# Optimization experiments

Hardware: AMD Instinct MI355X
Metric: run time of the kernel (lower is better)

## Reference

```python
import jax, jax.numpy as jnp
import numpy as np

N = 100000   # nodes
E = 800000   # edges
F_IN = 128   # in_channels
C = 64       # out_channels
H = 2 * C    # hidden = 2*out_channels


def _w(key, shape, fan_in):
    return jax.random.normal(key, shape, jnp.float32) * (1.0 / np.sqrt(fan_in))


def setup_inputs() -> dict:
    key = jax.random.key(0)
    ks = jax.random.split(key, 12)
    return {
        "x": jax.random.normal(ks[0], (N, F_IN), jnp.float32),
        "edge_index": jax.random.randint(ks[1], (2, E), 0, N, dtype=jnp.int32),
        # layer 1 (F_IN -> H)
        "W1_in": _w(ks[2], (F_IN, H), F_IN),
        "W1_out": _w(ks[3], (F_IN, H), F_IN),
        "W1_root": _w(ks[4], (F_IN, H), F_IN),
        "b1": jnp.zeros((H,), jnp.float32),
        # layer 2 (H -> C)
        "W2_in": _w(ks[5], (H, C), H),
        "W2_out": _w(ks[6], (H, C), H),
        "W2_root": _w(ks[7], (H, C), H),
        "b2": jnp.zeros((C,), jnp.float32),
    }


def _gcn(x, W, src, dst):
    # GCNConv with add_self_loops=False, bias=None:
    # out[dst] += deg^-1/2[src] * deg^-1/2[dst] * (x @ W)[src]
    h = x @ W
    deg = jax.ops.segment_sum(jnp.ones_like(dst, jnp.float32), dst, num_segments=N)
    dinv = jnp.where(deg > 0, jax.lax.rsqrt(jnp.maximum(deg, 1.0)), 0.0)
    norm = dinv[src] * dinv[dst]                 # [E]
    msg = h[src] * norm[:, None]                 # [E, F_out]
    return jax.ops.segment_sum(msg, dst, num_segments=N)


def _dir_layer(x, W_in, W_out, W_root, b, src, dst, alpha=0.5):
    x_in = _gcn(x, W_in, src, dst)               # original direction
    x_out = _gcn(x, W_out, dst, src)             # flipped edges
    return alpha * x_out + (1.0 - alpha) * x_in + x @ W_root + b


def reference(x, edge_index, W1_in, W1_out, W1_root, b1, W2_in, W2_out, W2_root, b2):
    src, dst = edge_index[0], edge_index[1]
    h = jax.nn.relu(_dir_layer(x, W1_in, W1_out, W1_root, b1, src, dst))
    return _dir_layer(h, W2_in, W2_out, W2_root, b2, src, dst)
```

## Files before the change

### kernel.cpp

```cpp
#include <hip/hip_runtime.h>

typedef __attribute__((ext_vector_type(8))) short bf16x8;
typedef __attribute__((ext_vector_type(4))) float f32x4;

#define NB 196
#define CAP 8192
#define SBLK 256
#define ECH 3125
#define GEMM_BLOCKS 1563

__device__ __forceinline__ unsigned short f2bf(float f) {
    unsigned int u = __float_as_uint(f);
    u = (u + 0x7FFFu + ((u >> 16) & 1u)) >> 16;
    return (unsigned short)u;
}
__device__ __forceinline__ float bf2f(unsigned short v) {
    return __uint_as_float(((unsigned int)v) << 16);
}

__device__ __forceinline__ void gemm1_body(
    unsigned short* As, unsigned short* Bs, int bid,
    const float* __restrict__ Ag, const unsigned short* __restrict__ BTcat,
    const float* __restrict__ bias,
    unsigned short* __restrict__ Y0, unsigned short* __restrict__ Y1,
    unsigned short* __restrict__ Y2, int nrows)
{
    const int t  = threadIdx.x;
    const int w  = t >> 6, l = t & 63;
    const int g  = l >> 4, li = l & 15;
    const int wr = w >> 1, wc = w & 1;
    const int row0 = bid * 64;

    #pragma unroll
    for (int i = 0; i < 4; ++i) {
        const int q   = t + 256 * i;
        const int row = q >> 4;
        const int ck  = q & 15;
        unsigned short o[8];
        if (row0 + row < nrows) {
            const f32x4* src = (const f32x4*)(Ag + (size_t)(row0 + row) * 128 + ck * 8);
            const f32x4 a = __builtin_nontemporal_load(src);
            const f32x4 b = __builtin_nontemporal_load(src + 1);
            o[0]=f2bf(a.x); o[1]=f2bf(a.y); o[2]=f2bf(a.z); o[3]=f2bf(a.w);
            o[4]=f2bf(b.x); o[5]=f2bf(b.y); o[6]=f2bf(b.z); o[7]=f2bf(b.w);
        } else {
            #pragma unroll
            for (int u = 0; u < 8; ++u) o[u] = 0;
        }
        *(int4*)&As[row * 128 + ((ck ^ (row & 7)) << 3)] = *(int4*)o;
    }

    #pragma unroll 1
    for (int wgt = 0; wgt < 3; ++wgt) {
        __syncthreads();
        {
            const int4* Bg = (const int4*)(BTcat + (size_t)wgt * 128 * 128);
            #pragma unroll
            for (int i = 0; i < 8; ++i) {
                const int q   = t + 256 * i;
                const int row = q >> 4;
                const int ck  = q & 15;
                const int4 v  = Bg[q];
                *(int4*)&Bs[row * 128 + ((ck ^ (row & 7)) << 3)] = v;
            }
        }
        __syncthreads();

        f32x4 acc[2][4];
        #pragma unroll
        for (int rf = 0; rf < 2; ++rf)
            #pragma unroll
            for (int cf = 0; cf < 4; ++cf)
                acc[rf][cf] = (f32x4){0.f, 0.f, 0.f, 0.f};

        #pragma unroll
        for (int kk = 0; kk < 4; ++kk) {
            bf16x8 av[2], bv[4];
            #pragma unroll
            for (int rf = 0; rf < 2; ++rf) {
                const int ar = wr * 32 + rf * 16 + li;
                const int ck = (kk * 4 + g) ^ (ar & 7);
                av[rf] = *(const bf16x8*)&As[ar * 128 + (ck << 3)];
            }
            #pragma unroll
            for (int cf = 0; cf < 4; ++cf) {
                const int bc = wc * 64 + cf * 16 + li;
                const int ck = (kk * 4 + g) ^ (bc & 7);
                bv[cf] = *(const bf16x8*)&Bs[bc * 128 + (ck << 3)];
            }
            #pragma unroll
            for (int rf = 0; rf < 2; ++rf)
                #pragma unroll
                for (int cf = 0; cf < 4; ++cf)
                    acc[rf][cf] = __builtin_amdgcn_mfma_f32_16x16x32_bf16(
                        av[rf], bv[cf], acc[rf][cf], 0, 0, 0);
        }

        unsigned short* Y = (wgt == 0) ? Y0 : (wgt == 1) ? Y1 : Y2;
        #pragma unroll
        for (int rf = 0; rf < 2; ++rf) {
            #pragma unroll
            for (int i = 0; i < 4; ++i) {
                const int r = row0 + wr * 32 + rf * 16 + 4 * g + i;
                if (r < nrows) {
                    #pragma unroll
                    for (int cf = 0; cf < 4; ++cf) {
                        const int c = wc * 64 + cf * 16 + li;
                        float v = acc[rf][cf][i];
                        if (wgt == 0) v += bias[c];
                        Y[(size_t)r * 128 + c] = f2bf(v);
                    }
                }
            }
        }
    }
}

__device__ __forceinline__ void bscatter_body(
    int* lds, int bid,
    const int* __restrict__ src, const int* __restrict__ dst,
    int* __restrict__ bcnt_in, int* __restrict__ bcnt_out,
    int* __restrict__ ebuf_in, int* __restrict__ ebuf_out, int E)
{
    int* lcnt_d  = lds;
    int* lcnt_s  = lds + NB;
    int* lbase_d = lds + 2 * NB;
    int* lbase_s = lds + 3 * NB;
    const int t = threadIdx.x;
    const int c0 = bid * ECH;
    const int c1 = min(E, c0 + ECH);
    for (int i = t; i < NB; i += 256) { lcnt_d[i] = 0; lcnt_s[i] = 0; }
    __syncthreads();
    for (int e = c0 + t; e < c1; e += 256) {
        atomicAdd(&lcnt_d[dst[e] >> 9], 1);
        atomicAdd(&lcnt_s[src[e] >> 9], 1);
    }
    __syncthreads();
    for (int b = t; b < NB; b += 256) {
        lbase_d[b] = atomicAdd(&bcnt_in[b],  lcnt_d[b]);
        lbase_s[b] = atomicAdd(&bcnt_out[b], lcnt_s[b]);
        lcnt_d[b] = 0; lcnt_s[b] = 0;
    }
    __syncthreads();
    for (int e = c0 + t; e < c1; e += 256) {
        const int s = src[e], d = dst[e];
        const int bd = d >> 9, bs = s >> 9;
        const int rd = atomicAdd(&lcnt_d[bd], 1);
        ebuf_in [bd * CAP + lbase_d[bd] + rd] = (s << 9) | (d & 511);
        const int rs = atomicAdd(&lcnt_s[bs], 1);
        ebuf_out[bs * CAP + lbase_s[bs] + rs] = (d << 9) | (s & 511);
    }
}

__global__ __launch_bounds__(256)
void fused1_k(const float* __restrict__ x, const unsigned short* __restrict__ wt1,
              const float* __restrict__ b1,
              unsigned short* __restrict__ y1b, unsigned short* __restrict__ h_in,
              unsigned short* __restrict__ h_out,
              const int* __restrict__ src, const int* __restrict__ dst,
              int* __restrict__ bcnt_in, int* __restrict__ bcnt_out,
              int* __restrict__ ebuf_in, int* __restrict__ ebuf_out,
              int nrows, int E)
{
    __shared__ unsigned short lds[64 * 128 + 128 * 128];
    if (blockIdx.x < SBLK) {
        bscatter_body((int*)lds, blockIdx.x,
                      src, dst, bcnt_in, bcnt_out, ebuf_in, ebuf_out, E);
    } else {
        gemm1_body(lds, lds + 64 * 128, blockIdx.x - SBLK,
                   x, wt1, b1, y1b, h_in, h_out, nrows);
    }
}

__global__ __launch_bounds__(256)
void gemm2_k(const unsigned short* __restrict__ Axb,
             const unsigned short* __restrict__ BTcat,
             const float* __restrict__ bias,
             const float* __restrict__ dinv_in, const float* __restrict__ dinv_out,
             unsigned short* __restrict__ Y0, unsigned short* __restrict__ Y1,
             unsigned short* __restrict__ Y2, int nrows)
{
    __shared__ unsigned short As[64 * 128];
    __shared__ unsigned short Bs[64 * 128];

    const int t  = threadIdx.x;
    const int w  = t >> 6, l = t & 63;
    const int g  = l >> 4, li = l & 15;
    const int wr = w >> 1, wc = w & 1;
    const int row0 = blockIdx.x * 64;

    {
        const int4* Ag = (const int4*)(Axb + (size_t)row0 * 128);
        #pragma unroll
        for (int i = 0; i < 4; ++i) {
            const int q   = t + 256 * i;
            const int row = q >> 4;
            const int ck  = q & 15;
            const int4 v  = Ag[q];
            *(int4*)&As[row * 128 + ((ck ^ (row & 7)) << 3)] = v;
        }
    }

    #pragma unroll 1
    for (int wgt = 0; wgt < 3; ++wgt) {
        __syncthreads();
        {
            const int4* Bg = (const int4*)(BTcat + (size_t)wgt * 64 * 128);
            #pragma unroll
            for (int i = 0; i < 4; ++i) {
                const int q   = t + 256 * i;
                const int row = q >> 4;
                const int ck  = q & 15;
                const int4 v  = Bg[q];
                *(int4*)&Bs[row * 128 + ((ck ^ (row & 7)) << 3)] = v;
            }
        }
        __syncthreads();

        f32x4 acc[2][2];
        #pragma unroll
        for (int rf = 0; rf < 2; ++rf)
            #pragma unroll
            for (int cf = 0; cf < 2; ++cf)
                acc[rf][cf] = (f32x4){0.f, 0.f, 0.f, 0.f};

        #pragma unroll
        for (int kk = 0; kk < 4; ++kk) {
            bf16x8 av[2], bv[2];
            #pragma unroll
            for (int rf = 0; rf < 2; ++rf) {
                const int ar = wr * 32 + rf * 16 + li;
                const int ck = (kk * 4 + g) ^ (ar & 7);
                av[rf] = *(const bf16x8*)&As[ar * 128 + (ck << 3)];
            }
            #pragma unroll
            for (int cf = 0; cf < 2; ++cf) {
                const int bc = wc * 32 + cf * 16 + li;
                const int ck = (kk * 4 + g) ^ (bc & 7);
                bv[cf] = *(const bf16x8*)&Bs[bc * 128 + (ck << 3)];
            }
            #pragma unroll
            for (int rf = 0; rf < 2; ++rf)
                #pragma unroll
                for (int cf = 0; cf < 2; ++cf)
                    acc[rf][cf] = __builtin_amdgcn_mfma_f32_16x16x32_bf16(
                        av[rf], bv[cf], acc[rf][cf], 0, 0, 0);
        }

        unsigned short* Y = (wgt == 0) ? Y0 : (wgt == 1) ? Y1 : Y2;
        const float* dv = (wgt == 1) ? dinv_in : dinv_out;
        #pragma unroll
        for (int rf = 0; rf < 2; ++rf) {
            #pragma unroll
            for (int i = 0; i < 4; ++i) {
                const int r = row0 + wr * 32 + rf * 16 + 4 * g + i;
                if (r < nrows) {
                    const float s = (wgt == 0) ? 1.f : 0.5f * dv[r];
                    #pragma unroll
                    for (int cf = 0; cf < 2; ++cf) {
                        const int c = wc * 32 + cf * 16 + li;
                        float v = acc[rf][cf][i];
                        v = (wgt == 0) ? (v + bias[c]) : (v * s);
                        Y[(size_t)r * 64 + c] = f2bf(v);
                    }
                }
            }
        }
    }
}

__global__ __launch_bounds__(256)
void wtrans_all_k(const float* __restrict__ W1r, const float* __restrict__ W1i,
                  const float* __restrict__ W1o, const float* __restrict__ W2r,
                  const float* __restrict__ W2i, const float* __restrict__ W2o,
                  unsigned short* __restrict__ T1, unsigned short* __restrict__ T2,
                  int* __restrict__ bcnt)
{
    const int tid = blockIdx.x * 256 + threadIdx.x;
    if (tid < 2 * NB) bcnt[tid] = 0;
    if (tid >= 3 * 16384 + 3 * 8192) return;
    const float* W; unsigned short* T; int M, r, base;
    if (tid < 49152) {
        const int w = tid / 16384; r = tid % 16384; M = 128;
        W = (w == 0) ? W1r : (w == 1) ? W1i : W1o;
        T = T1; base = w * 128;
    } else {
        const int u = tid - 49152;
        const int w = u / 8192; r = u % 8192; M = 64;
        W = (w == 0) ? W2r : (w == 1) ? W2i : W2o;
        T = T2; base = w * 64;
    }
    const int m = r & (M - 1);
    const int k = r / M;
    T[(size_t)(base + m) * 128 + k] = f2bf(W[(size_t)k * M + m]);
}

__global__ __launch_bounds__(512)
void bdegfill_k(const int* __restrict__ ebuf_in, const int* __restrict__ ebuf_out,
                const int* __restrict__ bcnt_in, const int* __restrict__ bcnt_out,
                float* __restrict__ dinv_in, float* __restrict__ dinv_out,
                int* __restrict__ rp_in, int* __restrict__ rp_out,
                int* __restrict__ col_in, int* __restrict__ col_out, int N, int E)
{
    __shared__ int cnt[512];
    __shared__ int cur[512];
    __shared__ int bsc[512];
    const int t = threadIdx.x;
    const int dir = (blockIdx.x >= NB) ? 1 : 0;
    const int b = blockIdx.x - dir * NB;
    const int* ebuf = dir ? ebuf_out : ebuf_in;
    const int* bcnt = dir ? bcnt_out : bcnt_in;

    bsc[t] = (t < NB) ? bcnt[t] : 0;
    __syncthreads();
    #pragma unroll
    for (int off = 1; off < 512; off <<= 1) {
        const int tv = (t >= off) ? bsc[t - off] : 0;
        __syncthreads();
        bsc[t] += tv;
        __syncthreads();
    }
    const int ne   = bcnt[b];
    const int base = bsc[b] - ne;
    const int e0 = b * CAP;

    cnt[t] = 0;
    __syncthreads();
    for (int j = t; j < ne; j += 512) atomicAdd(&cnt[ebuf[e0 + j] & 511], 1);
    __syncthreads();

    const int node = b * 512 + t;
    const int deg = cnt[t];
    float* dinv = dir ? dinv_out : dinv_in;
    if (node < N) dinv[node] = (deg > 0) ? rsqrtf((float)deg) : 0.f;

    #pragma unroll
    for (int off = 1; off < 512; off <<= 1) {
        const int tv = (t >= off) ? cnt[t - off] : 0;
        __syncthreads();
        cnt[t] += tv;
        __syncthreads();
    }
    int* rp = dir ? rp_out : rp_in;
    if (node < N) rp[node] = base + cnt[t] - deg;
    if (b == 0 && t == 0) rp[N] = E;
    cur[t] = cnt[t] - deg;
    __syncthreads();

    int* col = dir ? col_out : col_in;
    for (int j = t; j < ne; j += 512) {
        const int p = ebuf[e0 + j];
        const int slot = atomicAdd(&cur[p & 511], 1);
        col[base + slot] = p >> 9;
    }
}

template<bool EDGE_W>
__device__ __forceinline__ void accum8w(float* acc, const int4 v, float w) {
    const unsigned short* pp = (const unsigned short*)&v;
    #pragma unroll
    for (int u = 0; u < 8; ++u) {
        if (EDGE_W) acc[u] = fmaf(w, bf2f(pp[u]), acc[u]);
        else        acc[u] += bf2f(pp[u]);
    }
}

template<int F, bool RELU_BF16, bool EDGE_W>
__global__ __launch_bounds__(256)
void gather2_k(const unsigned short* __restrict__ h_in,
               const unsigned short* __restrict__ h_out,
               const int* __restrict__ rp_in,  const int* __restrict__ col_in,
               const int* __restrict__ rp_out, const int* __restrict__ col_out,
               const float* __restrict__ dinv_in, const float* __restrict__ dinv_out,
               const unsigned short* __restrict__ ybase, void* __restrict__ yout, int N)
{
    constexpr int TPN = F / 8;
    const int tid = blockIdx.x * 256 + threadIdx.x;
    const int n = tid / TPN;
    if (n >= N) return;
    const int c8 = (tid % TPN) * 8;

    const int bi = rp_in[n],  ei = rp_in[n + 1];
    const int bo = rp_out[n], eo = rp_out[n + 1];
    const float di = dinv_in[n], dq = dinv_out[n];
    const int4 yb4 = *(const int4*)(ybase + (size_t)n * F + c8);

    const unsigned short* hi = h_in + c8;
    const unsigned short* ho = h_out + c8;

    float acc_i[8] = {}, acc_o[8] = {};

    #pragma unroll 1
    for (int pass = 0; pass < 2; ++pass) {
        const int beg = pass ? bo : bi;
        const int end = pass ? eo : ei;
        const int* col = pass ? col_out : col_in;
        const float* dv = pass ? dinv_out : dinv_in;
        const unsigned short* h = pass ? ho : hi;
        float* acc = pass ? acc_o : acc_i;

        int j = beg;
        if (j + 4 <= end) {
            int c0 = col[j], c1 = col[j + 1], c2 = col[j + 2], c3 = col[j + 3];
            for (; j + 8 <= end; j += 4) {
                float w0 = 0.f, w1 = 0.f, w2 = 0.f, w3 = 0.f;
                if (EDGE_W) { w0 = dv[c0]; w1 = dv[c1]; w2 = dv[c2]; w3 = dv[c3]; }
                const int4 v0 = *(const int4*)(h + (size_t)c0 * F);
                const int4 v1 = *(const int4*)(h + (size_t)c1 * F);
                const int4 v2 = *(const int4*)(h + (size_t)c2 * F);
                const int4 v3 = *(const int4*)(h + (size_t)c3 * F);
                c0 = col[j + 4]; c1 = col[j + 5]; c2 = col[j + 6]; c3 = col[j + 7];
                accum8w<EDGE_W>(acc, v0, w0); accum8w<EDGE_W>(acc, v1, w1);
                accum8w<EDGE_W>(acc, v2, w2); accum8w<EDGE_W>(acc, v3, w3);
            }
            float w0 = 0.f, w1 = 0.f, w2 = 0.f, w3 = 0.f;
            if (EDGE_W) { w0 = dv[c0]; w1 = dv[c1]; w2 = dv[c2]; w3 = dv[c3]; }
            const int4 v0 = *(const int4*)(h + (size_t)c0 * F);
            const int4 v1 = *(const int4*)(h + (size_t)c1 * F);
            const int4 v2 = *(const int4*)(h + (size_t)c2 * F);
            const int4 v3 = *(const int4*)(h + (size_t)c3 * F);
            accum8w<EDGE_W>(acc, v0, w0); accum8w<EDGE_W>(acc, v1, w1);
            accum8w<EDGE_W>(acc, v2, w2); accum8w<EDGE_W>(acc, v3, w3);
            j += 4;
        }
        if (j < end) {
            const int rem = end - j;
            const int c0 = col[j];
            const int c1 = (rem > 1) ? col[j + 1] : c0;
            const int c2 = (rem > 2) ? col[j + 2] : c0;
            float w0 = 0.f, w1 = 0.f, w2 = 0.f;
            if (EDGE_W) { w0 = dv[c0]; w1 = dv[c1]; w2 = dv[c2]; }
            const int4 v0 = *(const int4*)(h + (size_t)c0 * F);
            if (rem > 1) {
                const int4 v1 = *(const int4*)(h + (size_t)c1 * F);
                accum8w<EDGE_W>(acc, v1, w1);
            }
            if (rem > 2) {
                const int4 v2 = *(const int4*)(h + (size_t)c2 * F);
                accum8w<EDGE_W>(acc, v2, w2);
            }
            accum8w<EDGE_W>(acc, v0, w0);
        }
    }

    const unsigned short* yb = (const unsigned short*)&yb4;
    const float si = EDGE_W ? 0.5f * di : di;
    const float sq = EDGE_W ? 0.5f * dq : dq;
    float v[8];
    #pragma unroll
    for (int u = 0; u < 8; ++u)
        v[u] = bf2f(yb[u]) + si * acc_i[u] + sq * acc_o[u];

    if (RELU_BF16) {
        unsigned short o[8];
        #pragma unroll
        for (int u = 0; u < 8; ++u) o[u] = f2bf(fmaxf(v[u], 0.f));
        *(int4*)((unsigned short*)yout + (size_t)n * F + c8) = *(int4*)o;
    } else {
        f32x4* yp = (f32x4*)((float*)yout + (size_t)n * F + c8);
        __builtin_nontemporal_store((f32x4){v[0], v[1], v[2], v[3]}, yp);
        __builtin_nontemporal_store((f32x4){v[4], v[5], v[6], v[7]}, yp + 1);
    }
}

extern "C" void kernel_launch(void* const* d_in, const int* in_sizes, int n_in,
                              void* d_out, int out_size, void* d_ws, size_t ws_size,
                              hipStream_t stream)
{
    const int N = 100000, E = 800000, C = 64, H = 128;
    const int Npad = ((N + 63) / 64) * 64;

    const float* x       = (const float*)d_in[0];
    const int*   ei      = (const int*)d_in[1];
    const int*   src     = ei;
    const int*   dst     = ei + E;
    const float* W1_in   = (const float*)d_in[2];
    const float* W1_out  = (const float*)d_in[3];
    const float* W1_root = (const float*)d_in[4];
    const float* b1      = (const float*)d_in[5];
    const float* W2_in   = (const float*)d_in[6];
    const float* W2_out  = (const float*)d_in[7];
    const float* W2_root = (const float*)d_in[8];
    const float* b2      = (const float*)d_in[9];
    float* out = (float*)d_out;

    char* p = (char*)d_ws;
    int*   bcnt_in  = (int*)p;            p += (size_t)(2 * NB + 8) * 4;
    int*   bcnt_out = bcnt_in + NB;
    float* dinv_in  = (float*)p;          p += (size_t)N * 4;
    float* dinv_out = (float*)p;          p += (size_t)N * 4;
    int*   rp_in    = (int*)p;            p += (size_t)(N + 8) * 4;
    int*   rp_out   = (int*)p;            p += (size_t)(N + 8) * 4;
    int*   col_in   = (int*)p;            p += (size_t)E * 4;
    int*   col_out  = (int*)p;            p += (size_t)E * 4;
    int*   ebuf_in  = (int*)p;            p += (size_t)NB * CAP * 4;
    int*   ebuf_out = (int*)p;            p += (size_t)NB * CAP * 4;
    unsigned short* wt1 = (unsigned short*)p;       p += (size_t)384 * 128 * 2;
    unsigned short* wt2 = (unsigned short*)p;       p += (size_t)192 * 128 * 2;
    unsigned short* xb  = (unsigned short*)p;       p += (size_t)Npad * 128 * 2;
    unsigned short* y1b = (unsigned short*)p;       p += (size_t)Npad * 128 * 2;
    unsigned short* h_in = (unsigned short*)p;      p += (size_t)Npad * 128 * 2;
    unsigned short* h_out= (unsigned short*)p;      p += (size_t)Npad * 128 * 2;

    const dim3 blk(256);

    wtrans_all_k<<<288, blk, 0, stream>>>(W1_root, W1_in, W1_out, W2_root, W2_in, W2_out,
                                          wt1, wt2, bcnt_in);

    fused1_k<<<SBLK + GEMM_BLOCKS, blk, 0, stream>>>(
        x, wt1, b1, y1b, h_in, h_out,
        src, dst, bcnt_in, bcnt_out, ebuf_in, ebuf_out, N, E);

    bdegfill_k<<<2 * NB, 512, 0, stream>>>(ebuf_in, ebuf_out, bcnt_in, bcnt_out,
                                           dinv_in, dinv_out,
                                           rp_in, rp_out, col_in, col_out, N, E);

    const int ga1 = (N * (H / 8) + 255) / 256;
    const int ga2 = (N * (C / 8) + 255) / 256;

    gather2_k<128, true, true><<<ga1, blk, 0, stream>>>(
        h_in, h_out, rp_in, col_in, rp_out, col_out,
        dinv_in, dinv_out, y1b, xb, N);

    gemm2_k<<<GEMM_BLOCKS, blk, 0, stream>>>(
        xb, wt2, b2, dinv_in, dinv_out, y1b, h_in, h_out, N);
    gather2_k<64, false, false><<<ga2, blk, 0, stream>>>(
        h_in, h_out, rp_in, col_in, rp_out, col_out,
        dinv_in, dinv_out, y1b, out, N);
}
```

Measured before the change: 215.9 us.

## Fuse layer-1 gather with layer-2 GEMM into one kernel

Merges the layer-1 aggregation (with ReLU and bf16 cast) and the layer-2 three-way projection into a single kernel. Each block gathers 16 nodes into LDS, then runs MFMA against the whole 192x128 layer-2 weight held in LDS. This removes the round trip of the intermediate activation through global memory and one kernel launch. In exchange every block reloads 48KB of weights into LDS, which lowers occupancy, and the layer-2 root output is written into the reused edge buffer. The final gather is split into its own non-templated kernel.

```diff
diff --git a/kernel.cpp b/kernel.cpp
--- a/kernel.cpp
+++ b/kernel.cpp
@@ -169,103 +169,6 @@
     } else {
         gemm1_body(lds, lds + 64 * 128, blockIdx.x - SBLK,
                    x, wt1, b1, y1b, h_in, h_out, nrows);
-    }
-}
-
-__global__ __launch_bounds__(256)
-void gemm2_k(const unsigned short* __restrict__ Axb,
-             const unsigned short* __restrict__ BTcat,
-             const float* __restrict__ bias,
-             const float* __restrict__ dinv_in, const float* __restrict__ dinv_out,
-             unsigned short* __restrict__ Y0, unsigned short* __restrict__ Y1,
-             unsigned short* __restrict__ Y2, int nrows)
-{
-    __shared__ unsigned short As[64 * 128];
-    __shared__ unsigned short Bs[64 * 128];
-
-    const int t  = threadIdx.x;
-    const int w  = t >> 6, l = t & 63;
-    const int g  = l >> 4, li = l & 15;
-    const int wr = w >> 1, wc = w & 1;
-    const int row0 = blockIdx.x * 64;
-
-    {
-        const int4* Ag = (const int4*)(Axb + (size_t)row0 * 128);
-        #pragma unroll
-        for (int i = 0; i < 4; ++i) {
-            const int q   = t + 256 * i;
-            const int row = q >> 4;
-            const int ck  = q & 15;
-            const int4 v  = Ag[q];
-            *(int4*)&As[row * 128 + ((ck ^ (row & 7)) << 3)] = v;
-        }
-    }
-
-    #pragma unroll 1
-    for (int wgt = 0; wgt < 3; ++wgt) {
-        __syncthreads();
-        {
-            const int4* Bg = (const int4*)(BTcat + (size_t)wgt * 64 * 128);
-            #pragma unroll
-            for (int i = 0; i < 4; ++i) {
-                const int q   = t + 256 * i;
-                const int row = q >> 4;
-                const int ck  = q & 15;
-                const int4 v  = Bg[q];
-                *(int4*)&Bs[row * 128 + ((ck ^ (row & 7)) << 3)] = v;
-            }
-        }
-        __syncthreads();
-
-        f32x4 acc[2][2];
-        #pragma unroll
-        for (int rf = 0; rf < 2; ++rf)
-            #pragma unroll
-            for (int cf = 0; cf < 2; ++cf)
-                acc[rf][cf] = (f32x4){0.f, 0.f, 0.f, 0.f};
-
-        #pragma unroll
-        for (int kk = 0; kk < 4; ++kk) {
-            bf16x8 av[2], bv[2];
-            #pragma unroll
-            for (int rf = 0; rf < 2; ++rf) {
-                const int ar = wr * 32 + rf * 16 + li;
-                const int ck = (kk * 4 + g) ^ (ar & 7);
-                av[rf] = *(const bf16x8*)&As[ar * 128 + (ck << 3)];
-            }
-            #pragma unroll
-            for (int cf = 0; cf < 2; ++cf) {
-                const int bc = wc * 32 + cf * 16 + li;
-                const int ck = (kk * 4 + g) ^ (bc & 7);
-                bv[cf] = *(const bf16x8*)&Bs[bc * 128 + (ck << 3)];
-            }
-            #pragma unroll
-            for (int rf = 0; rf < 2; ++rf)
-                #pragma unroll
-                for (int cf = 0; cf < 2; ++cf)
-                    acc[rf][cf] = __builtin_amdgcn_mfma_f32_16x16x32_bf16(
-                        av[rf], bv[cf], acc[rf][cf], 0, 0, 0);
-        }
-
-        unsigned short* Y = (wgt == 0) ? Y0 : (wgt == 1) ? Y1 : Y2;
-        const float* dv = (wgt == 1) ? dinv_in : dinv_out;
-        #pragma unroll
-        for (int rf = 0; rf < 2; ++rf) {
-            #pragma unroll
-            for (int i = 0; i < 4; ++i) {
-                const int r = row0 + wr * 32 + rf * 16 + 4 * g + i;
-                if (r < nrows) {
-                    const float s = (wgt == 0) ? 1.f : 0.5f * dv[r];
-                    #pragma unroll
-                    for (int cf = 0; cf < 2; ++cf) {
-                        const int c = wc * 32 + cf * 16 + li;
-                        float v = acc[rf][cf][i];
-                        v = (wgt == 0) ? (v + bias[c]) : (v * s);
-                        Y[(size_t)r * 64 + c] = f2bf(v);
-                    }
-                }
-            }
-        }
     }
 }
 
@@ -365,25 +268,43 @@
     }
 }
 
-template<int F, bool RELU_BF16, bool EDGE_W>
 __global__ __launch_bounds__(256)
-void gather2_k(const unsigned short* __restrict__ h_in,
+void gfused2_k(const unsigned short* __restrict__ h_in,
                const unsigned short* __restrict__ h_out,
                const int* __restrict__ rp_in,  const int* __restrict__ col_in,
                const int* __restrict__ rp_out, const int* __restrict__ col_out,
                const float* __restrict__ dinv_in, const float* __restrict__ dinv_out,
-               const unsigned short* __restrict__ ybase, void* __restrict__ yout, int N)
-{
-    constexpr int TPN = F / 8;
-    const int tid = blockIdx.x * 256 + threadIdx.x;
-    const int n = tid / TPN;
-    if (n >= N) return;
-    const int c8 = (tid % TPN) * 8;
+               const unsigned short* __restrict__ ybase,
+               const unsigned short* __restrict__ wt2,
+               const float* __restrict__ b2,
+               unsigned short* __restrict__ y2b,
+               unsigned short* __restrict__ h2_in,
+               unsigned short* __restrict__ h2_out)
+{
+    __shared__ unsigned short xs[16 * 128];
+    __shared__ unsigned short Bs[192 * 128];
+
+    const int t  = threadIdx.x;
+    const int ln = t >> 4;
+    const int n  = blockIdx.x * 16 + ln;
+    const int c8 = (t & 15) * 8;
+
+    {
+        const int4* Bg = (const int4*)wt2;
+        #pragma unroll
+        for (int i = 0; i < 12; ++i) {
+            const int q   = t + 256 * i;
+            const int row = q >> 4;
+            const int ck  = q & 15;
+            const int4 v  = Bg[q];
+            *(int4*)&Bs[row * 128 + ((ck ^ (row & 7)) << 3)] = v;
+        }
+    }
 
     const int bi = rp_in[n],  ei = rp_in[n + 1];
     const int bo = rp_out[n], eo = rp_out[n + 1];
     const float di = dinv_in[n], dq = dinv_out[n];
-    const int4 yb4 = *(const int4*)(ybase + (size_t)n * F + c8);
+    const int4 yb4 = *(const int4*)(ybase + (size_t)n * 128 + c8);
 
     const unsigned short* hi = h_in + c8;
     const unsigned short* ho = h_out + c8;
@@ -403,24 +324,149 @@
         if (j + 4 <= end) {
             int c0 = col[j], c1 = col[j + 1], c2 = col[j + 2], c3 = col[j + 3];
             for (; j + 8 <= end; j += 4) {
-                float w0 = 0.f, w1 = 0.f, w2 = 0.f, w3 = 0.f;
-                if (EDGE_W) { w0 = dv[c0]; w1 = dv[c1]; w2 = dv[c2]; w3 = dv[c3]; }
+                const float w0 = dv[c0], w1 = dv[c1], w2 = dv[c2], w3 = dv[c3];
+                const int4 v0 = *(const int4*)(h + (size_t)c0 * 128);
+                const int4 v1 = *(const int4*)(h + (size_t)c1 * 128);
+                const int4 v2 = *(const int4*)(h + (size_t)c2 * 128);
+                const int4 v3 = *(const int4*)(h + (size_t)c3 * 128);
+                c0 = col[j + 4]; c1 = col[j + 5]; c2 = col[j + 6]; c3 = col[j + 7];
+                accum8w<true>(acc, v0, w0); accum8w<true>(acc, v1, w1);
+                accum8w<true>(acc, v2, w2); accum8w<true>(acc, v3, w3);
+            }
+            const float w0 = dv[c0], w1 = dv[c1], w2 = dv[c2], w3 = dv[c3];
+            const int4 v0 = *(const int4*)(h + (size_t)c0 * 128);
+            const int4 v1 = *(const int4*)(h + (size_t)c1 * 128);
+            const int4 v2 = *(const int4*)(h + (size_t)c2 * 128);
+            const int4 v3 = *(const int4*)(h + (size_t)c3 * 128);
+            accum8w<true>(acc, v0, w0); accum8w<true>(acc, v1, w1);
+            accum8w<true>(acc, v2, w2); accum8w<true>(acc, v3, w3);
+            j += 4;
+        }
+        if (j < end) {
+            const int rem = end - j;
+            const int c0 = col[j];
+            const int c1 = (rem > 1) ? col[j + 1] : c0;
+            const int c2 = (rem > 2) ? col[j + 2] : c0;
+            const float w0 = dv[c0], w1 = dv[c1], w2 = dv[c2];
+            const int4 v0 = *(const int4*)(h + (size_t)c0 * 128);
+            if (rem > 1) {
+                const int4 v1 = *(const int4*)(h + (size_t)c1 * 128);
+                accum8w<true>(acc, v1, w1);
+            }
+            if (rem > 2) {
+                const int4 v2 = *(const int4*)(h + (size_t)c2 * 128);
+                accum8w<true>(acc, v2, w2);
+            }
+            accum8w<true>(acc, v0, w0);
+        }
+    }
+
+    {
+        const unsigned short* yb = (const unsigned short*)&yb4;
+        const float si = 0.5f * di, sq = 0.5f * dq;
+        unsigned short o[8];
+        #pragma unroll
+        for (int u = 0; u < 8; ++u) {
+            const float v = bf2f(yb[u]) + si * acc_i[u] + sq * acc_o[u];
+            o[u] = f2bf(fmaxf(v, 0.f));
+        }
+        *(int4*)&xs[ln * 128 + (((t & 15) ^ (ln & 7)) << 3)] = *(int4*)o;
+    }
+
+    __syncthreads();
+
+    const int w = t >> 6, l = t & 63;
+    const int g = l >> 4, li = l & 15;
+
+    f32x4 acc2[3];
+    #pragma unroll
+    for (int cf = 0; cf < 3; ++cf) acc2[cf] = (f32x4){0.f, 0.f, 0.f, 0.f};
+
+    #pragma unroll
+    for (int kk = 0; kk < 4; ++kk) {
+        const int cka = (kk * 4 + g) ^ (li & 7);
+        const bf16x8 av = *(const bf16x8*)&xs[li * 128 + (cka << 3)];
+        bf16x8 bv[3];
+        #pragma unroll
+        for (int cf = 0; cf < 3; ++cf) {
+            const int bc = w * 48 + cf * 16 + li;
+            const int ck = (kk * 4 + g) ^ (bc & 7);
+            bv[cf] = *(const bf16x8*)&Bs[bc * 128 + (ck << 3)];
+        }
+        #pragma unroll
+        for (int cf = 0; cf < 3; ++cf)
+            acc2[cf] = __builtin_amdgcn_mfma_f32_16x16x32_bf16(av, bv[cf], acc2[cf], 0, 0, 0);
+    }
+
+    #pragma unroll
+    for (int cf = 0; cf < 3; ++cf) {
+        const int c   = w * 48 + cf * 16 + li;
+        const int sel = c >> 6;
+        const int cc  = c & 63;
+        #pragma unroll
+        for (int i = 0; i < 4; ++i) {
+            const int node = blockIdx.x * 16 + 4 * g + i;
+            const float vv = acc2[cf][i];
+            if (sel == 0)
+                y2b[(size_t)node * 64 + cc] = f2bf(vv + b2[cc]);
+            else if (sel == 1)
+                h2_in[(size_t)node * 64 + cc] = f2bf(vv * 0.5f * dinv_in[node]);
+            else
+                h2_out[(size_t)node * 64 + cc] = f2bf(vv * 0.5f * dinv_out[node]);
+        }
+    }
+}
+
+__global__ __launch_bounds__(256)
+void gatherf_k(const unsigned short* __restrict__ h2_in,
+               const unsigned short* __restrict__ h2_out,
+               const int* __restrict__ rp_in,  const int* __restrict__ col_in,
+               const int* __restrict__ rp_out, const int* __restrict__ col_out,
+               const float* __restrict__ dinv_in, const float* __restrict__ dinv_out,
+               const unsigned short* __restrict__ ybase, float* __restrict__ yout, int N)
+{
+    constexpr int F = 64, TPN = 8;
+    const int tid = blockIdx.x * 256 + threadIdx.x;
+    const int n = tid / TPN;
+    if (n >= N) return;
+    const int c8 = (tid % TPN) * 8;
+
+    const int bi = rp_in[n],  ei = rp_in[n + 1];
+    const int bo = rp_out[n], eo = rp_out[n + 1];
+    const float di = dinv_in[n], dq = dinv_out[n];
+    const int4 yb4 = *(const int4*)(ybase + (size_t)n * F + c8);
+
+    const unsigned short* hi = h2_in + c8;
+    const unsigned short* ho = h2_out + c8;
+
+    float acc_i[8] = {}, acc_o[8] = {};
+
+    #pragma unroll 1
+    for (int pass = 0; pass < 2; ++pass) {
+        const int beg = pass ? bo : bi;
+        const int end = pass ? eo : ei;
+        const int* col = pass ? col_out : col_in;
+        const unsigned short* h = pass ? ho : hi;
+        float* acc = pass ? acc_o : acc_i;
+
+        int j = beg;
+        if (j + 4 <= end) {
+            int c0 = col[j], c1 = col[j + 1], c2 = col[j + 2], c3 = col[j + 3];
+            for (; j + 8 <= end; j += 4) {
                 const int4 v0 = *(const int4*)(h + (size_t)c0 * F);
                 const int4 v1 = *(const int4*)(h + (size_t)c1 * F);
                 const int4 v2 = *(const int4*)(h + (size_t)c2 * F);
                 const int4 v3 = *(const int4*)(h + (size_t)c3 * F);
                 c0 = col[j + 4]; c1 = col[j + 5]; c2 = col[j + 6]; c3 = col[j + 7];
-                accum8w<EDGE_W>(acc, v0, w0); accum8w<EDGE_W>(acc, v1, w1);
-                accum8w<EDGE_W>(acc, v2, w2); accum8w<EDGE_W>(acc, v3, w3);
-            }
-            float w0 = 0.f, w1 = 0.f, w2 = 0.f, w3 = 0.f;
-            if (EDGE_W) { w0 = dv[c0]; w1 = dv[c1]; w2 = dv[c2]; w3 = dv[c3]; }
+                accum8w<false>(acc, v0, 0.f); accum8w<false>(acc, v1, 0.f);
+                accum8w<false>(acc, v2, 0.f); accum8w<false>(acc, v3, 0.f);
+            }
             const int4 v0 = *(const int4*)(h + (size_t)c0 * F);
             const int4 v1 = *(const int4*)(h + (size_t)c1 * F);
             const int4 v2 = *(const int4*)(h + (size_t)c2 * F);
             const int4 v3 = *(const int4*)(h + (size_t)c3 * F);
-            accum8w<EDGE_W>(acc, v0, w0); accum8w<EDGE_W>(acc, v1, w1);
-            accum8w<EDGE_W>(acc, v2, w2); accum8w<EDGE_W>(acc, v3, w3);
+            accum8w<false>(acc, v0, 0.f); accum8w<false>(acc, v1, 0.f);
+            accum8w<false>(acc, v2, 0.f); accum8w<false>(acc, v3, 0.f);
             j += 4;
         }
         if (j < end) {
@@ -428,39 +474,28 @@
             const int c0 = col[j];
             const int c1 = (rem > 1) ? col[j + 1] : c0;
             const int c2 = (rem > 2) ? col[j + 2] : c0;
-            float w0 = 0.f, w1 = 0.f, w2 = 0.f;
-            if (EDGE_W) { w0 = dv[c0]; w1 = dv[c1]; w2 = dv[c2]; }
             const int4 v0 = *(const int4*)(h + (size_t)c0 * F);
             if (rem > 1) {
                 const int4 v1 = *(const int4*)(h + (size_t)c1 * F);
-                accum8w<EDGE_W>(acc, v1, w1);
+                accum8w<false>(acc, v1, 0.f);
             }
             if (rem > 2) {
                 const int4 v2 = *(const int4*)(h + (size_t)c2 * F);
-                accum8w<EDGE_W>(acc, v2, w2);
-            }
-            accum8w<EDGE_W>(acc, v0, w0);
+                accum8w<false>(acc, v2, 0.f);
+            }
+            accum8w<false>(acc, v0, 0.f);
         }
     }
 
     const unsigned short* yb = (const unsigned short*)&yb4;
-    const float si = EDGE_W ? 0.5f * di : di;
-    const float sq = EDGE_W ? 0.5f * dq : dq;
     float v[8];
     #pragma unroll
     for (int u = 0; u < 8; ++u)
-        v[u] = bf2f(yb[u]) + si * acc_i[u] + sq * acc_o[u];
-
-    if (RELU_BF16) {
-        unsigned short o[8];
-        #pragma unroll
-        for (int u = 0; u < 8; ++u) o[u] = f2bf(fmaxf(v[u], 0.f));
-        *(int4*)((unsigned short*)yout + (size_t)n * F + c8) = *(int4*)o;
-    } else {
-        f32x4* yp = (f32x4*)((float*)yout + (size_t)n * F + c8);
-        __builtin_nontemporal_store((f32x4){v[0], v[1], v[2], v[3]}, yp);
-        __builtin_nontemporal_store((f32x4){v[4], v[5], v[6], v[7]}, yp + 1);
-    }
+        v[u] = bf2f(yb[u]) + di * acc_i[u] + dq * acc_o[u];
+
+    f32x4* yp = (f32x4*)(yout + (size_t)n * F + c8);
+    __builtin_nontemporal_store((f32x4){v[0], v[1], v[2], v[3]}, yp);
+    __builtin_nontemporal_store((f32x4){v[4], v[5], v[6], v[7]}, yp + 1);
 }
 
 extern "C" void kernel_launch(void* const* d_in, const int* in_sizes, int n_in,
@@ -497,11 +532,15 @@
     int*   ebuf_out = (int*)p;            p += (size_t)NB * CAP * 4;
     unsigned short* wt1 = (unsigned short*)p;       p += (size_t)384 * 128 * 2;
     unsigned short* wt2 = (unsigned short*)p;       p += (size_t)192 * 128 * 2;
-    unsigned short* xb  = (unsigned short*)p;       p += (size_t)Npad * 128 * 2;
+    unsigned short* h2buf = (unsigned short*)p;     p += (size_t)Npad * 128 * 2;
     unsigned short* y1b = (unsigned short*)p;       p += (size_t)Npad * 128 * 2;
     unsigned short* h_in = (unsigned short*)p;      p += (size_t)Npad * 128 * 2;
     unsigned short* h_out= (unsigned short*)p;      p += (size_t)Npad * 128 * 2;
 
+    unsigned short* y2b   = (unsigned short*)ebuf_in;
+    unsigned short* h2_in  = h2buf;
+    unsigned short* h2_out = h2buf + (size_t)Npad * 64;
+
     const dim3 blk(256);
 
     wtrans_all_k<<<288, blk, 0, stream>>>(W1_root, W1_in, W1_out, W2_root, W2_in, W2_out,
@@ -515,16 +554,12 @@
                                            dinv_in, dinv_out,
                                            rp_in, rp_out, col_in, col_out, N, E);
 
-    const int ga1 = (N * (H / 8) + 255) / 256;
+    gfused2_k<<<N / 16, blk, 0, stream>>>(
+        h_in, h_out, rp_in, col_in, rp_out, col_out,
+        dinv_in, dinv_out, y1b, wt2, b2, y2b, h2_in, h2_out);
+
     const int ga2 = (N * (C / 8) + 255) / 256;
-
-    gather2_k<128, true, true><<<ga1, blk, 0, stream>>>(
-        h_in, h_out, rp_in, col_in, rp_out, col_out,
-        dinv_in, dinv_out, y1b, xb, N);
-
-    gemm2_k<<<GEMM_BLOCKS, blk, 0, stream>>>(
-        xb, wt2, b2, dinv_in, dinv_out, y1b, h_in, h_out, N);
-    gather2_k<64, false, false><<<ga2, blk, 0, stream>>>(
-        h_in, h_out, rp_in, col_in, rp_out, col_out,
-        dinv_in, dinv_out, y1b, out, N);
-}
+    gatherf_k<<<ga2, blk, 0, stream>>>(
+        h2_in, h2_out, rp_in, col_in, rp_out, col_out,
+        dinv_in, dinv_out, y2b, out, N);
+}
```

Measured after the change: 225.5 us. 4.5% more time.
